# Performance work log

Hardware: AMD Instinct MI355X
Metric: run time of the kernel (lower is better)

The kernel has to match this reference:

```python
import jax, jax.numpy as jnp
import numpy as np

SEQ, D_IN, D_OUT = 8192, 768, 768

def setup_inputs() -> dict:
    key = jax.random.key(0)
    k1, k2, k3, k4 = jax.random.split(key, 4)
    scale = 1.0 / np.sqrt(D_IN)
    return {
        "x": jax.random.normal(k1, (SEQ, D_IN), dtype=jnp.float32),
        "w_q": jax.random.normal(k2, (D_OUT, D_IN), dtype=jnp.float32) * scale,
        "w_k": jax.random.normal(k3, (D_OUT, D_IN), dtype=jnp.float32) * scale,
        "w_v": jax.random.normal(k4, (D_OUT, D_IN), dtype=jnp.float32) * scale,
    }

def reference(x, w_q, w_k, w_v):
    # torch Linear: y = x @ W.T (no bias since qkv_bias=False)
    q = x @ w_q.T  # [S, D]
    k = x @ w_k.T  # [S, D]
    v = x @ w_v.T  # [S, D]
    scores = (q @ k.T) / jnp.sqrt(jnp.asarray(k.shape[-1], x.dtype))  # [S, S]
    attn = jax.nn.softmax(scores, axis=-1)
    return attn @ v  # [S, D]
```

## Files before the change

kernel.cpp:

```cpp
#include <hip/hip_runtime.h>

#define SEQ 8192
#define DIM 768

typedef __attribute__((ext_vector_type(8))) short s16x8;
typedef __attribute__((ext_vector_type(4))) float f32x4;

__device__ __forceinline__ unsigned short f2bf(float f) {
  union { float f; unsigned u; } v; v.f = f;
  unsigned r = v.u + 0x7FFFu + ((v.u >> 16) & 1u);
  return (unsigned short)(r >> 16);
}

__device__ __forceinline__ float bf2f(unsigned short s) {
  union { unsigned u; float f; } v; v.u = ((unsigned)s) << 16;
  return v.f;
}

__device__ __forceinline__ void gll16(const void* gsrc, void* ldst) {
  __builtin_amdgcn_global_load_lds(
      (__attribute__((address_space(1))) unsigned int*)gsrc,
      (__attribute__((address_space(3))) unsigned int*)ldst, 16, 0, 0);
}

#define XN4 (SEQ * DIM / 4)
#define WN4 (DIM * DIM / 4)

__global__ void cast_all_kernel(const float* __restrict__ x, const float* __restrict__ wq,
                                const float* __restrict__ wk, const float* __restrict__ wv,
                                unsigned short* __restrict__ dx, unsigned short* __restrict__ dq,
                                unsigned short* __restrict__ dk, unsigned short* __restrict__ dv) {
  int i = blockIdx.x * blockDim.x + threadIdx.x;
  const float* s;
  unsigned short* d;
  int off;
  if (i < XN4) {
    s = x; d = dx; off = i;
  } else {
    int j = i - XN4;
    int wi = j / WN4;
    off = j - wi * WN4;
    s = (wi == 0) ? wq : ((wi == 1) ? wk : wv);
    d = (wi == 0) ? dq : ((wi == 1) ? dk : dv);
  }
  float4 v = ((const float4*)s)[off];
  ushort4 r; r.x = f2bf(v.x); r.y = f2bf(v.y); r.z = f2bf(v.z); r.w = f2bf(v.w);
  ((ushort4*)d)[off] = r;
}

__global__ __launch_bounds__(256, 2)
void proj_kernel(const unsigned short* __restrict__ X,
                 const unsigned short* __restrict__ Wq,
                 const unsigned short* __restrict__ Wk,
                 const unsigned short* __restrict__ Wv,
                 unsigned short* __restrict__ Qb,
                 unsigned short* __restrict__ Kb,
                 unsigned short* __restrict__ Vtb) {
  __shared__ __align__(16) char lds[65536];
  const int tid = threadIdx.x;
  const int lane = tid & 63, wv = tid >> 6;
  const int l15 = lane & 15, l4 = lane >> 4;
  const int mt = blockIdx.x, nt = blockIdx.y, z = blockIdx.z;
  const unsigned short* W = (z == 0) ? Wq : ((z == 1) ? Wk : Wv);

  f32x4 acc[4][4];
#pragma unroll
  for (int i = 0; i < 4; ++i)
#pragma unroll
    for (int j = 0; j < 4; ++j) acc[i][j] = f32x4{0.f, 0.f, 0.f, 0.f};

  auto stage = [&](int kk) {
    char* At = lds + (kk & 1) * 32768;
    char* Bt = At + 16384;
    const int d0 = kk * 64;
#pragma unroll
    for (int i = 0; i < 4; ++i) {
      int s = i * 256 + tid;
      int row = s >> 3, c = (s & 7) ^ (row & 7);
      gll16(X + (long)(mt * 128 + row) * DIM + d0 + c * 8, At + i * 4096 + (wv << 10));
      gll16(W + (long)(nt * 128 + row) * DIM + d0 + c * 8, Bt + i * 4096 + (wv << 10));
    }
  };

  stage(0);
#pragma unroll 1
  for (int kk = 0; kk < 12; ++kk) {
    __syncthreads();
    if (kk + 1 < 12) stage(kk + 1);
    const char* At = lds + (kk & 1) * 32768;
    const char* Bt = At + 16384;
#pragma unroll
    for (int ks = 0; ks < 2; ++ks) {
      const int c = ks * 4 + l4;
      s16x8 a[4], b[4];
#pragma unroll
      for (int mi = 0; mi < 4; ++mi) {
        int row = (wv & 1) * 64 + mi * 16 + l15;
        a[mi] = *(const s16x8*)(At + row * 128 + ((c ^ (row & 7)) << 4));
      }
#pragma unroll
      for (int ni = 0; ni < 4; ++ni) {
        int row = (wv >> 1) * 64 + ni * 16 + l15;
        b[ni] = *(const s16x8*)(Bt + row * 128 + ((c ^ (row & 7)) << 4));
      }
#pragma unroll
      for (int mi = 0; mi < 4; ++mi)
#pragma unroll
        for (int ni = 0; ni < 4; ++ni)
          acc[mi][ni] = __builtin_amdgcn_mfma_f32_16x16x32_bf16(a[mi], b[ni], acc[mi][ni], 0, 0, 0);
    }
  }

#pragma unroll
  for (int mi = 0; mi < 4; ++mi)
#pragma unroll
    for (int ni = 0; ni < 4; ++ni) {
      int row0 = mt * 128 + (wv & 1) * 64 + mi * 16 + l4 * 4;
      int col = nt * 128 + (wv >> 1) * 64 + ni * 16 + l15;
      if (z == 2) {
        ushort4 r;
        r.x = f2bf(acc[mi][ni][0]); r.y = f2bf(acc[mi][ni][1]);
        r.z = f2bf(acc[mi][ni][2]); r.w = f2bf(acc[mi][ni][3]);
        *(ushort4*)(Vtb + (long)col * SEQ + row0) = r;
      } else {
        unsigned short* dst = (z == 0) ? Qb : Kb;
#pragma unroll
        for (int g = 0; g < 4; ++g)
          dst[(long)(row0 + g) * DIM + col] = f2bf(acc[mi][ni][g]);
      }
    }
}

#define SCALE_LOG2E 0.05205878f

__global__ __launch_bounds__(512, 2)
void flash_kernel(const unsigned short* __restrict__ Q,
                  const unsigned short* __restrict__ K,
                  const unsigned short* __restrict__ V,
                  unsigned short* __restrict__ partp,
                  float* __restrict__ outf,
                  float* __restrict__ lout,
                  int kv_len, int norm_out) {
  __shared__ __align__(16) char lds[80 * 1024 + 32 * 1024 + 1024];
  char* arena = lds;
  char* Pl = lds + 81920;
  float* l_part = (float*)(lds + 81920 + 32768);

  const int tid = threadIdx.x;
  const int lane = tid & 63, wv = tid >> 6;
  const int l15 = lane & 15, l4 = lane >> 4;
  const int qtile = blockIdx.x, split = blockIdx.y;
  const long kv0 = (long)split * kv_len;
  const long qrow0 = (long)qtile * 64;
  const int R = wv & 1;
  const int C = wv >> 1;

  f32x4 acc_o[4][6];
  float acc_lp[8];
#pragma unroll
  for (int i = 0; i < 4; ++i)
#pragma unroll
    for (int j = 0; j < 6; ++j) acc_o[i][j] = f32x4{0.f, 0.f, 0.f, 0.f};
#pragma unroll
  for (int i = 0; i < 8; ++i) acc_lp[i] = 0.f;

  const int niter = kv_len >> 8;

#pragma unroll 1
  for (int it = 0; it < niter; ++it) {
    const long kb = kv0 + (long)it * 256;

    auto stageQK = [&](int r) {
      char* Qc = arena + (r & 1) * 40960;
      char* Kc = Qc + 8192;
      const int d0 = r * 64;
      {
        int s = tid;
        int row = s >> 3, c = (s & 7) ^ (row & 7);
        gll16(Q + (qrow0 + row) * DIM + d0 + c * 8, Qc + (wv << 10));
      }
#pragma unroll
      for (int i = 0; i < 4; ++i) {
        int s = i * 512 + tid;
        int row = s >> 3, c = (s & 7) ^ (row & 7);
        gll16(K + (kb + row) * DIM + d0 + c * 8, Kc + i * 8192 + (wv << 10));
      }
    };
    auto stagePV = [&](int r) {
      char* Vc = arena + (r & 1) * 32768;
      const int cc_ = r >> 2, kh_ = r & 3;
#pragma unroll
      for (int i = 0; i < 4; ++i) {
        int s = i * 512 + tid;
        int vr = s >> 3, c = (s & 7) ^ (vr & 7);
        gll16(V + (long)(cc_ * 256 + vr) * SEQ + kb + kh_ * 64 + c * 8, Vc + i * 8192 + (wv << 10));
      }
    };

    f32x4 acc_s[2][4];
#pragma unroll
    for (int a = 0; a < 2; ++a)
#pragma unroll
      for (int b = 0; b < 4; ++b) acc_s[a][b] = f32x4{0.f, 0.f, 0.f, 0.f};

    stageQK(0);
#pragma unroll 1
    for (int r = 0; r < 12; ++r) {
      __syncthreads();
      if (r + 1 < 12) stageQK(r + 1);
      const char* Qc = arena + (r & 1) * 40960;
      const char* Kc = Qc + 8192;
#pragma unroll
      for (int ks = 0; ks < 2; ++ks) {
        const int c = ks * 4 + l4;
        s16x8 af[2], bk[4];
#pragma unroll
        for (int rt = 0; rt < 2; ++rt) {
          int row = R * 32 + rt * 16 + l15;
          af[rt] = *(const s16x8*)(Qc + row * 128 + ((c ^ (row & 7)) << 4));
        }
#pragma unroll
        for (int ct = 0; ct < 4; ++ct) {
          int kr = C * 64 + ct * 16 + l15;
          bk[ct] = *(const s16x8*)(Kc + kr * 128 + ((c ^ (kr & 7)) << 4));
        }
#pragma unroll
        for (int rt = 0; rt < 2; ++rt)
#pragma unroll
          for (int ct = 0; ct < 4; ++ct)
            acc_s[rt][ct] = __builtin_amdgcn_mfma_f32_16x16x32_bf16(af[rt], bk[ct], acc_s[rt][ct], 0, 0, 0);
      }
    }

#pragma unroll
    for (int rt = 0; rt < 2; ++rt)
#pragma unroll
      for (int ct = 0; ct < 4; ++ct)
#pragma unroll
        for (int g = 0; g < 4; ++g) {
          float p = exp2f(acc_s[rt][ct][g] * SCALE_LOG2E);
          acc_lp[rt * 4 + g] += p;
          int row = R * 32 + rt * 16 + l4 * 4 + g;
          int col = C * 64 + ct * 16 + l15;
          int off = row * 512 + ((((col >> 3) ^ (row & 7))) << 4) + ((col & 7) << 1);
          *(unsigned short*)(Pl + off) = f2bf(p);
        }

    stagePV(0);
#pragma unroll
    for (int cc = 0; cc < 3; ++cc) {
#pragma unroll 1
      for (int kh = 0; kh < 4; ++kh) {
        const int r = cc * 4 + kh;
        __syncthreads();
        if (r + 1 < 12) stagePV(r + 1);
        const char* Vc = arena + (r & 1) * 32768;
#pragma unroll
        for (int ks = 0; ks < 2; ++ks) {
          s16x8 pa[4], vb[2];
          const int ck = kh * 8 + ks * 4 + l4;
#pragma unroll
          for (int rs = 0; rs < 4; ++rs) {
            int row = rs * 16 + l15;
            int pc = (ck & ~7) | ((ck & 7) ^ (row & 7));
            pa[rs] = *(const s16x8*)(Pl + row * 512 + (pc << 4));
          }
          const int cv = ks * 4 + l4;
#pragma unroll
          for (int t = 0; t < 2; ++t) {
            int vr = (wv + 8 * t) * 16 + l15;
            vb[t] = *(const s16x8*)(Vc + vr * 128 + ((cv ^ (vr & 7)) << 4));
          }
#pragma unroll
          for (int rs = 0; rs < 4; ++rs)
#pragma unroll
            for (int t = 0; t < 2; ++t)
              acc_o[rs][cc * 2 + t] =
                  __builtin_amdgcn_mfma_f32_16x16x32_bf16(pa[rs], vb[t], acc_o[rs][cc * 2 + t], 0, 0, 0);
        }
      }
    }
    __syncthreads();
  }

#pragma unroll
  for (int i = 0; i < 8; ++i) {
    float v = acc_lp[i];
    v += __shfl_xor(v, 1); v += __shfl_xor(v, 2);
    v += __shfl_xor(v, 4); v += __shfl_xor(v, 8);
    acc_lp[i] = v;
  }
  if (l15 == 0) {
#pragma unroll
    for (int rt = 0; rt < 2; ++rt)
#pragma unroll
      for (int g = 0; g < 4; ++g)
        l_part[C * 64 + R * 32 + rt * 16 + l4 * 4 + g] = acc_lp[rt * 4 + g];
  }
  __syncthreads();

  if (!norm_out) {
    if (tid < 64)
      lout[(long)split * SEQ + qrow0 + tid] =
          l_part[tid] + l_part[64 + tid] + l_part[128 + tid] + l_part[192 + tid];
#pragma unroll
    for (int rt = 0; rt < 4; ++rt) {
      int row = rt * 16 + l4 * 4;
#pragma unroll
      for (int j = 0; j < 6; ++j) {
        int cc = j >> 1, t = j & 1;
        int col = (cc * 16 + wv + 8 * t) * 16 + l15;
#pragma unroll
        for (int g = 0; g < 4; ++g)
          partp[(long)split * SEQ * DIM + (qrow0 + row + g) * DIM + col] = f2bf(acc_o[rt][j][g]);
      }
    }
  } else {
    float linv[4][4];
#pragma unroll
    for (int rt = 0; rt < 4; ++rt)
#pragma unroll
      for (int g = 0; g < 4; ++g) {
        int row = rt * 16 + l4 * 4 + g;
        linv[rt][g] = 1.0f / (l_part[row] + l_part[64 + row] + l_part[128 + row] + l_part[192 + row]);
      }
#pragma unroll
    for (int rt = 0; rt < 4; ++rt) {
      int row = rt * 16 + l4 * 4;
#pragma unroll
      for (int j = 0; j < 6; ++j) {
        int cc = j >> 1, t = j & 1;
        int col = (cc * 16 + wv + 8 * t) * 16 + l15;
#pragma unroll
        for (int g = 0; g < 4; ++g)
          outf[(qrow0 + row + g) * DIM + col] = acc_o[rt][j][g] * linv[rt][g];
      }
    }
  }
}

__global__ void combine_kernel(const unsigned short* __restrict__ part,
                               const float* __restrict__ lsum,
                               float* __restrict__ out, int n4) {
  int i = blockIdx.x * blockDim.x + threadIdx.x;
  if (i >= n4) return;
  int row = (i * 4) / DIM;
  ushort4 p0 = ((const ushort4*)part)[i];
  ushort4 p1 = ((const ushort4*)(part + (long)SEQ * DIM))[i];
  float inv = 1.0f / (lsum[row] + lsum[SEQ + row]);
  float4 o;
  o.x = (bf2f(p0.x) + bf2f(p1.x)) * inv;
  o.y = (bf2f(p0.y) + bf2f(p1.y)) * inv;
  o.z = (bf2f(p0.z) + bf2f(p1.z)) * inv;
  o.w = (bf2f(p0.w) + bf2f(p1.w)) * inv;
  ((float4*)out)[i] = o;
}

extern "C" void kernel_launch(void* const* d_in, const int* in_sizes, int n_in,
                              void* d_out, int out_size, void* d_ws, size_t ws_size,
                              hipStream_t stream) {
  const float* x = (const float*)d_in[0];
  const float* wq = (const float*)d_in[1];
  const float* wk = (const float*)d_in[2];
  const float* wv = (const float*)d_in[3];
  float* out = (float*)d_out;
  char* ws = (char*)d_ws;

  const size_t o_xbf = 0;
  const size_t o_wq = o_xbf + (size_t)SEQ * DIM * 2;
  const size_t o_wk = o_wq + (size_t)DIM * DIM * 2;
  const size_t o_wv = o_wk + (size_t)DIM * DIM * 2;
  const size_t o_q = o_wv + (size_t)DIM * DIM * 2;
  const size_t o_k = o_q + (size_t)SEQ * DIM * 2;
  const size_t o_vt = o_k + (size_t)SEQ * DIM * 2;
  const size_t o_part = o_vt + (size_t)SEQ * DIM * 2;
  const size_t o_l = o_part + (size_t)2 * SEQ * DIM * 2;
  const size_t total_g2 = o_l + (size_t)2 * SEQ * 4;

  unsigned short* Xbf = (unsigned short*)(ws + o_xbf);
  unsigned short* Wqb = (unsigned short*)(ws + o_wq);
  unsigned short* Wkb = (unsigned short*)(ws + o_wk);
  unsigned short* Wvb = (unsigned short*)(ws + o_wv);
  unsigned short* Qb = (unsigned short*)(ws + o_q);
  unsigned short* Kb = (unsigned short*)(ws + o_k);
  unsigned short* Vtb = (unsigned short*)(ws + o_vt);
  unsigned short* part = (unsigned short*)(ws + o_part);
  float* lbuf = (float*)(ws + o_l);

  const int G = (ws_size >= total_g2) ? 2 : 1;

  cast_all_kernel<<<7872, 256, 0, stream>>>(x, wq, wk, wv, Xbf, Wqb, Wkb, Wvb);
  proj_kernel<<<dim3(64, 6, 3), 256, 0, stream>>>(Xbf, Wqb, Wkb, Wvb, Qb, Kb, Vtb);
  if (G == 2) {
    flash_kernel<<<dim3(128, 2), 512, 0, stream>>>(Qb, Kb, Vtb, part, nullptr, lbuf, SEQ / 2, 0);
    combine_kernel<<<6144, 256, 0, stream>>>(part, lbuf, out, SEQ * DIM / 4);
  } else {
    flash_kernel<<<dim3(128, 1), 512, 0, stream>>>(Qb, Kb, Vtb, nullptr, out, nullptr, SEQ, 1);
  }
}
```

Before: 332.0 us.

## Block V in 32-key tiles and overlap V and next-Q/K prefetch across phases

```diff
diff --git a/kernel.cpp b/kernel.cpp
--- a/kernel.cpp
+++ b/kernel.cpp
@@ -121,7 +121,7 @@
         ushort4 r;
         r.x = f2bf(acc[mi][ni][0]); r.y = f2bf(acc[mi][ni][1]);
         r.z = f2bf(acc[mi][ni][2]); r.w = f2bf(acc[mi][ni][3]);
-        *(ushort4*)(Vtb + (long)col * SEQ + row0) = r;
+        *(ushort4*)(Vtb + (long)(row0 >> 5) * (DIM * 32) + col * 32 + (row0 & 31)) = r;
       } else {
         unsigned short* dst = (z == 0) ? Qb : Kb;
 #pragma unroll
@@ -141,10 +141,9 @@
                   float* __restrict__ outf,
                   float* __restrict__ lout,
                   int kv_len, int norm_out) {
-  __shared__ __align__(16) char lds[80 * 1024 + 32 * 1024 + 1024];
-  char* arena = lds;
-  char* Pl = lds + 81920;
-  float* l_part = (float*)(lds + 81920 + 32768);
+  __shared__ __align__(16) char lds[131072];
+  char* Pl = lds + 98304;
+  float* l_part = (float*)lds;
 
   const int tid = threadIdx.x;
   const int lane = tid & 63, wv = tid >> 6;
@@ -166,36 +165,47 @@
 
   const int niter = kv_len >> 8;
 
+  auto vchunk = [&](int par, int j) -> char* {
+    int base = par ? ((j < 5) ? 40960 + j * 8192 : 90112)
+                   : ((j < 5) ? j * 8192 : 81920);
+    return lds + base;
+  };
+
+  auto stageQK = [&](int r, long kbase) {
+    char* Qc = lds + (r & 1) * 40960;
+    char* Kc = Qc + 8192;
+    const int d0 = r * 64;
+    {
+      int s = tid;
+      int row = s >> 3, c = (s & 7) ^ (row & 7);
+      gll16(Q + (qrow0 + row) * DIM + d0 + c * 8, Qc + (wv << 10));
+    }
+#pragma unroll
+    for (int i = 0; i < 4; ++i) {
+      int s = i * 512 + tid;
+      int row = s >> 3, c = (s & 7) ^ (row & 7);
+      gll16(K + (kbase + row) * DIM + d0 + c * 8, Kc + i * 8192 + (wv << 10));
+    }
+  };
+
+  auto stagePV = [&](int v, long kblk0) {
+    const int par = v & 1;
+    const long blkbase = (kblk0 + v) * (long)(DIM * 32);
+    int s = wv * 64 + lane;
+    int rp = s >> 3, p3 = s & 7;
+    int orig = p3 ^ (rp & 7);
+    int vr_in = rp * 2 + (orig >> 2);
+    int k4 = orig & 3;
+#pragma unroll
+    for (int i = 0; i < 6; ++i)
+      gll16(V + blkbase + (long)(i * 128 + vr_in) * 32 + k4 * 8, vchunk(par, i) + (wv << 10));
+  };
+
+  stageQK(0, kv0);
 #pragma unroll 1
   for (int it = 0; it < niter; ++it) {
     const long kb = kv0 + (long)it * 256;
-
-    auto stageQK = [&](int r) {
-      char* Qc = arena + (r & 1) * 40960;
-      char* Kc = Qc + 8192;
-      const int d0 = r * 64;
-      {
-        int s = tid;
-        int row = s >> 3, c = (s & 7) ^ (row & 7);
-        gll16(Q + (qrow0 + row) * DIM + d0 + c * 8, Qc + (wv << 10));
-      }
-#pragma unroll
-      for (int i = 0; i < 4; ++i) {
-        int s = i * 512 + tid;
-        int row = s >> 3, c = (s & 7) ^ (row & 7);
-        gll16(K + (kb + row) * DIM + d0 + c * 8, Kc + i * 8192 + (wv << 10));
-      }
-    };
-    auto stagePV = [&](int r) {
-      char* Vc = arena + (r & 1) * 32768;
-      const int cc_ = r >> 2, kh_ = r & 3;
-#pragma unroll
-      for (int i = 0; i < 4; ++i) {
-        int s = i * 512 + tid;
-        int vr = s >> 3, c = (s & 7) ^ (vr & 7);
-        gll16(V + (long)(cc_ * 256 + vr) * SEQ + kb + kh_ * 64 + c * 8, Vc + i * 8192 + (wv << 10));
-      }
-    };
+    const long kblk0 = kb >> 5;
 
     f32x4 acc_s[2][4];
 #pragma unroll
@@ -203,12 +213,12 @@
 #pragma unroll
       for (int b = 0; b < 4; ++b) acc_s[a][b] = f32x4{0.f, 0.f, 0.f, 0.f};
 
-    stageQK(0);
 #pragma unroll 1
     for (int r = 0; r < 12; ++r) {
       __syncthreads();
-      if (r + 1 < 12) stageQK(r + 1);
-      const char* Qc = arena + (r & 1) * 40960;
+      if (r + 1 < 12) stageQK(r + 1, kb);
+      else stagePV(0, kblk0);
+      const char* Qc = lds + (r & 1) * 40960;
       const char* Kc = Qc + 8192;
 #pragma unroll
       for (int ks = 0; ks < 2; ++ks) {
@@ -246,41 +256,35 @@
           *(unsigned short*)(Pl + off) = f2bf(p);
         }
 
-    stagePV(0);
-#pragma unroll
-    for (int cc = 0; cc < 3; ++cc) {
 #pragma unroll 1
-      for (int kh = 0; kh < 4; ++kh) {
-        const int r = cc * 4 + kh;
-        __syncthreads();
-        if (r + 1 < 12) stagePV(r + 1);
-        const char* Vc = arena + (r & 1) * 32768;
-#pragma unroll
-        for (int ks = 0; ks < 2; ++ks) {
-          s16x8 pa[4], vb[2];
-          const int ck = kh * 8 + ks * 4 + l4;
-#pragma unroll
-          for (int rs = 0; rs < 4; ++rs) {
-            int row = rs * 16 + l15;
-            int pc = (ck & ~7) | ((ck & 7) ^ (row & 7));
-            pa[rs] = *(const s16x8*)(Pl + row * 512 + (pc << 4));
-          }
-          const int cv = ks * 4 + l4;
-#pragma unroll
-          for (int t = 0; t < 2; ++t) {
-            int vr = (wv + 8 * t) * 16 + l15;
-            vb[t] = *(const s16x8*)(Vc + vr * 128 + ((cv ^ (vr & 7)) << 4));
-          }
+    for (int v = 0; v < 8; ++v) {
+      __syncthreads();
+      if (v + 1 < 8) stagePV(v + 1, kblk0);
+      else if (it + 1 < niter) stageQK(0, kb + 256);
+      const int par = v & 1;
+      s16x8 pa[4];
+      const int ck = v * 4 + l4;
+#pragma unroll
+      for (int rs = 0; rs < 4; ++rs) {
+        int row = rs * 16 + l15;
+        int pc = (ck & ~7) | ((ck & 7) ^ (row & 7));
+        pa[rs] = *(const s16x8*)(Pl + row * 512 + (pc << 4));
+      }
+      const int vr_l = wv * 16 + l15;
+      const int rp = vr_l >> 1;
+      const int p3 = (((l15 & 1) << 2) | l4) ^ (rp & 7);
+#pragma unroll
+      for (int cc = 0; cc < 3; ++cc)
+#pragma unroll
+        for (int t = 0; t < 2; ++t) {
+          const char* vcb = vchunk(par, cc * 2 + t);
+          s16x8 vb = *(const s16x8*)(vcb + rp * 128 + (p3 << 4));
 #pragma unroll
           for (int rs = 0; rs < 4; ++rs)
-#pragma unroll
-            for (int t = 0; t < 2; ++t)
-              acc_o[rs][cc * 2 + t] =
-                  __builtin_amdgcn_mfma_f32_16x16x32_bf16(pa[rs], vb[t], acc_o[rs][cc * 2 + t], 0, 0, 0);
+            acc_o[rs][cc * 2 + t] =
+                __builtin_amdgcn_mfma_f32_16x16x32_bf16(pa[rs], vb, acc_o[rs][cc * 2 + t], 0, 0, 0);
         }
-      }
-    }
-    __syncthreads();
+    }
   }
 
 #pragma unroll
@@ -290,6 +294,7 @@
     v += __shfl_xor(v, 4); v += __shfl_xor(v, 8);
     acc_lp[i] = v;
   }
+  __syncthreads();
   if (l15 == 0) {
 #pragma unroll
     for (int rt = 0; rt < 2; ++rt)
```

Result: faster. 316.4 us (-4.7%).
